# Performance work log

Measured on AMD Instinct MI355X. Metric: run time of the kernel, lower is better.

The kernel has to match this reference:

```python
import jax, jax.numpy as jnp
import numpy as np

C = 256
CQK = C // 8  # query/key channel dim from Conv3d(in, in//8, 1)


def setup_inputs() -> dict:
    key = jax.random.key(0)
    ks = jax.random.split(key, 8)
    B, D, H, W = 2, 16, 16, 16
    x = jax.random.normal(ks[0], (B, C, D, H, W), dtype=jnp.float32)
    s = 1.0 / np.sqrt(C)
    q_w = jax.random.normal(ks[1], (CQK, C), dtype=jnp.float32) * s
    q_b = jax.random.normal(ks[2], (CQK,), dtype=jnp.float32) * 0.01
    k_w = jax.random.normal(ks[3], (CQK, C), dtype=jnp.float32) * s
    k_b = jax.random.normal(ks[4], (CQK,), dtype=jnp.float32) * 0.01
    v_w = jax.random.normal(ks[5], (C, C), dtype=jnp.float32) * s
    v_b = jax.random.normal(ks[6], (C,), dtype=jnp.float32) * 0.01
    gamma = jax.random.normal(ks[7], (1,), dtype=jnp.float32)
    return {"x": x, "q_w": q_w, "q_b": q_b, "k_w": k_w, "k_b": k_b,
            "v_w": v_w, "v_b": v_b, "gamma": gamma}


def reference(x, q_w, q_b, k_w, k_b, v_w, v_b, gamma):
    B, Cc, D, H, W = x.shape
    N = D * H * W
    xf = x.reshape(B, Cc, N)  # [B, C, N]
    # 1x1x1 Conv3d == channel-mixing matmul
    q = jnp.einsum('oc,bcn->bon', q_w, xf) + q_b[None, :, None]  # [B, C/8, N]
    k = jnp.einsum('oc,bcn->bon', k_w, xf) + k_b[None, :, None]  # [B, C/8, N]
    v = jnp.einsum('oc,bcn->bon', v_w, xf) + v_b[None, :, None]  # [B, C, N]
    # attention[b, i, j] = sum_c q[b, c, i] * k[b, c, j]
    attn = jnp.einsum('bci,bcj->bij', q, k)  # [B, N, N]
    attn = jax.nn.softmax(attn, axis=-1)
    # out[b, c, i] = sum_j v[b, c, j] * attn[b, i, j]
    out = jnp.einsum('bcj,bij->bci', v, attn)  # [B, C, N]
    out = out.reshape(B, Cc, D, H, W)
    return gamma[0] * out + x
```

## Files before the change

kernel.cpp:

```cpp
#include <hip/hip_runtime.h>

#define C_DIM 256
#define CQK   32
#define N_DIM 4096
#define B_DIM 2

typedef __attribute__((ext_vector_type(8))) short bf16x8;
typedef __attribute__((ext_vector_type(4))) float f32x4;

__device__ __forceinline__ unsigned short f2bf(float f) {
    union { float f; unsigned u; } v; v.f = f;
    unsigned r = v.u + 0x7FFFu + ((v.u >> 16) & 1u);
    return (unsigned short)(r >> 16);
}
__device__ __forceinline__ unsigned pk2(float a, float b) {
    return (unsigned)f2bf(a) | ((unsigned)f2bf(b) << 16);
}
#define MFMA(A, B, C) __builtin_amdgcn_mfma_f32_16x16x32_bf16((A), (B), (C), 0, 0, 0)

__global__ __launch_bounds__(256) void wconv(
    const float* __restrict__ q_w, const float* __restrict__ q_b,
    const float* __restrict__ k_w, const float* __restrict__ k_b,
    const float* __restrict__ v_w, const float* __restrict__ v_b,
    unsigned short* __restrict__ wbf, float* __restrict__ biasf)
{
    int o = blockIdx.x, c = threadIdx.x;
    float w;
    if (o < 32)       w = q_w[o * C_DIM + c];
    else if (o < 64)  w = k_w[(o - 32) * C_DIM + c];
    else              w = v_w[(o - 64) * C_DIM + c];
    wbf[o * C_DIM + c] = f2bf(w);
    if (c == 0) biasf[o] = (o < 32) ? q_b[o] : (o < 64) ? k_b[o - 32] : v_b[o - 64];
}

__global__ __launch_bounds__(256, 2) void qkv_proj(
    const float* __restrict__ x, const unsigned short* __restrict__ wbf,
    const float* __restrict__ biasf,
    unsigned short* __restrict__ qT, unsigned short* __restrict__ kT,
    unsigned short* __restrict__ vbf)
{
    __shared__ __align__(16) unsigned short xsT[16 * 264];
    __shared__ __align__(16) unsigned short qkbuf[2][16 * 36];
    __shared__ __align__(16) unsigned short vbb[256 * 20];
    const int t  = threadIdx.x;
    const int b  = blockIdx.x >> 8;
    const int n0 = (blockIdx.x & 255) * 16;

    {
        int n4 = t & 3, cq = t >> 2;
        const float* xp = x + ((size_t)(b * C_DIM + cq * 4)) * N_DIM + n0 + n4 * 4;
        float4 r0 = *(const float4*)xp;
        float4 r1 = *(const float4*)(xp + N_DIM);
        float4 r2 = *(const float4*)(xp + 2 * N_DIM);
        float4 r3 = *(const float4*)(xp + 3 * N_DIM);
        float a0[4], a1[4], a2[4], a3[4];
        *(float4*)a0 = r0; *(float4*)a1 = r1; *(float4*)a2 = r2; *(float4*)a3 = r3;
        #pragma unroll
        for (int k = 0; k < 4; ++k) {
            uint2 pw;
            pw.x = pk2(a0[k], a1[k]);
            pw.y = pk2(a2[k], a3[k]);
            *(uint2*)&xsT[(n4 * 4 + k) * 264 + cq * 4] = pw;
        }
    }
    __syncthreads();

    const int w = t >> 6, lid = t & 63, lr = lid & 15, lq = lid >> 4;
    f32x4 acc[5] = {};
    #pragma unroll
    for (int ks = 0; ks < 8; ++ks) {
        bf16x8 xb = *(const bf16x8*)&xsT[lr * 264 + ks * 32 + lq * 8];
        #pragma unroll
        for (int u = 0; u < 5; ++u) {
            int gm = w * 5 + u;
            bf16x8 af = *(const bf16x8*)&wbf[(gm * 16 + lr) * C_DIM + ks * 32 + lq * 8];
            acc[u] = MFMA(af, xb, acc[u]);
        }
    }
    #pragma unroll
    for (int u = 0; u < 5; ++u) {
        int gm = w * 5 + u;
        float bv[4];
        *(float4*)bv = *(const float4*)&biasf[gm * 16 + lq * 4];
        if (gm >= 4) {
            int vc = (gm - 4) * 16 + lq * 4;
            #pragma unroll
            for (int r = 0; r < 4; ++r)
                vbb[(vc + r) * 20 + lr] = f2bf(acc[u][r] + bv[r]);
        } else {
            int sel = gm >> 1, half = gm & 1;
            uint2 pw;
            pw.x = pk2(acc[u][0] + bv[0], acc[u][1] + bv[1]);
            pw.y = pk2(acc[u][2] + bv[2], acc[u][3] + bv[3]);
            *(uint2*)&qkbuf[sel][lr * 36 + half * 16 + lq * 4] = pw;
        }
    }
    __syncthreads();
    if (t < 128) {
        int sel = t >> 6, idx = t & 63;
        int n = idx >> 2, ch8 = (idx & 3) * 8;
        const unsigned short* src = &qkbuf[sel][n * 36 + ch8];
        uint2 a = *(const uint2*)src;
        uint2 c = *(const uint2*)(src + 4);
        unsigned short* dst = (sel ? kT : qT) + ((size_t)b * N_DIM + n0 + n) * CQK + ch8;
        uint4 st; st.x = a.x; st.y = a.y; st.z = c.x; st.w = c.y;
        *(uint4*)dst = st;
    }
    {
        const unsigned short* src = &vbb[t * 20];
        uint2 a = *(const uint2*)(src + 0);
        uint2 bq = *(const uint2*)(src + 4);
        uint2 c = *(const uint2*)(src + 8);
        uint2 d = *(const uint2*)(src + 12);
        unsigned short* dst = vbf + ((size_t)b * C_DIM + t) * N_DIM + n0;
        uint4 s0; s0.x = a.x; s0.y = a.y; s0.z = bq.x; s0.w = bq.y;
        uint4 s1; s1.x = c.x; s1.y = c.y; s1.z = d.x; s1.w = d.y;
        *(uint4*)dst = s0;
        *(uint4*)(dst + 8) = s1;
    }
}

__global__ __launch_bounds__(256, 2) void attn_kernel(
    const unsigned short* __restrict__ qT, const unsigned short* __restrict__ kT,
    const unsigned short* __restrict__ vbf, const float* __restrict__ x,
    const float* __restrict__ gamma, float* __restrict__ out)
{
    __shared__ __align__(16) char smem[20480 + 1280];
    unsigned short* pbase = (unsigned short*)smem;
    float* obuf = (float*)smem;
    float* lbuf = (float*)(smem + 20480);

    const int t  = threadIdx.x;
    const int b  = blockIdx.x >> 8;
    const int qt = (blockIdx.x >> 2) & 63;
    const int cs = blockIdx.x & 3;
    const int i0 = qt * 64, c0 = cs * 64;
    const int w = t >> 6, lid = t & 63, lr = lid & 15, lq = lid >> 4;

    const unsigned short* qTb = qT + (size_t)b * N_DIM * CQK;
    const unsigned short* kTb = kT + (size_t)b * N_DIM * CQK;
    const unsigned short* vb  = vbf + (size_t)b * C_DIM * N_DIM;

    unsigned short* pW = pbase + w * (64 * 40);

    bf16x8 bq[4];
    #pragma unroll
    for (int it = 0; it < 4; ++it)
        bq[it] = *(const bf16x8*)&qTb[(i0 + it * 16 + lr) * CQK + lq * 8];

    f32x4 oa[4][4] = {};
    float lp[4] = {};

    const int jwbase = w * 1024;
    #pragma unroll 2
    for (int jj = 0; jj < 1024; jj += 32) {
        const int j0 = jwbase + jj;
        bf16x8 ak0 = *(const bf16x8*)&kTb[(j0 + lr) * CQK + lq * 8];
        bf16x8 ak1 = *(const bf16x8*)&kTb[(j0 + 16 + lr) * CQK + lq * 8];
        bf16x8 av[4];
        #pragma unroll
        for (int ct = 0; ct < 4; ++ct)
            av[ct] = *(const bf16x8*)&vb[(size_t)(c0 + ct * 16 + lr) * N_DIM + j0 + lq * 8];

        const f32x4 z = {};
        #pragma unroll
        for (int it = 0; it < 4; ++it) {
            f32x4 s0 = MFMA(ak0, bq[it], z);
            f32x4 s1 = MFMA(ak1, bq[it], z);
            float e0 = __expf(s0[0]), e1 = __expf(s0[1]), e2 = __expf(s0[2]), e3 = __expf(s0[3]);
            float f0 = __expf(s1[0]), f1 = __expf(s1[1]), f2 = __expf(s1[2]), f3 = __expf(s1[3]);
            lp[it] += ((e0 + e1) + (e2 + e3)) + ((f0 + f1) + (f2 + f3));
            uint2 pw0; pw0.x = pk2(e0, e1); pw0.y = pk2(e2, e3);
            uint2 pw1; pw1.x = pk2(f0, f1); pw1.y = pk2(f2, f3);
            unsigned short* prow = pW + (it * 16 + lr) * 40;
            *(uint2*)&prow[lq * 4]      = pw0;
            *(uint2*)&prow[16 + lq * 4] = pw1;
        }
        __asm__ __volatile__("" ::: "memory");
        #pragma unroll
        for (int it = 0; it < 4; ++it) {
            bf16x8 bp = *(const bf16x8*)&pW[(it * 16 + lr) * 40 + lq * 8];
            #pragma unroll
            for (int ct = 0; ct < 4; ++ct)
                oa[ct][it] = MFMA(av[ct], bp, oa[ct][it]);
        }
    }

    #pragma unroll
    for (int it = 0; it < 4; ++it) {
        lp[it] += __shfl_xor(lp[it], 16);
        lp[it] += __shfl_xor(lp[it], 32);
    }
    if (lq == 0) {
        #pragma unroll
        for (int it = 0; it < 4; ++it)
            lbuf[w * 64 + it * 16 + lr] = lp[it];
    }
    __syncthreads();

    for (int ph = 0; ph < 4; ++ph) {
        if (w == ph) {
            #pragma unroll
            for (int ct = 0; ct < 4; ++ct)
                #pragma unroll
                for (int it = 0; it < 4; ++it)
                    #pragma unroll
                    for (int r = 0; r < 4; ++r) {
                        int addr = (ct * 16 + lq * 4 + r) * 68 + it * 16 + lr;
                        if (ph == 0) obuf[addr]  = oa[ct][it][r];
                        else         obuf[addr] += oa[ct][it][r];
                    }
        }
        __syncthreads();
    }
    if (t < 64) {
        float l = lbuf[t] + lbuf[64 + t] + lbuf[128 + t] + lbuf[192 + t];
        lbuf[256 + t] = 1.f / l;
    }
    __syncthreads();

    const float g = gamma[0];
    const int cc = t >> 2;
    const int ic = (t & 3) * 16;
    const size_t rowbase = ((size_t)b * C_DIM + c0 + cc) * N_DIM + i0 + ic;
    #pragma unroll
    for (int k = 0; k < 4; ++k) {
        float4 ov4 = *(const float4*)&obuf[cc * 68 + ic + k * 4];
        float4 li  = *(const float4*)&lbuf[256 + ic + k * 4];
        float4 xv  = *(const float4*)(x + rowbase + k * 4);
        float4 ov;
        ov.x = g * ov4.x * li.x + xv.x;
        ov.y = g * ov4.y * li.y + xv.y;
        ov.z = g * ov4.z * li.z + xv.z;
        ov.w = g * ov4.w * li.w + xv.w;
        *(float4*)(out + rowbase + k * 4) = ov;
    }
}

extern "C" void kernel_launch(void* const* d_in, const int* in_sizes, int n_in,
                              void* d_out, int out_size, void* d_ws, size_t ws_size,
                              hipStream_t stream) {
    const float* x     = (const float*)d_in[0];
    const float* q_w   = (const float*)d_in[1];
    const float* q_b   = (const float*)d_in[2];
    const float* k_w   = (const float*)d_in[3];
    const float* k_b   = (const float*)d_in[4];
    const float* v_w   = (const float*)d_in[5];
    const float* v_b   = (const float*)d_in[6];
    const float* gamma = (const float*)d_in[7];
    float* out = (float*)d_out;

    char* ws = (char*)d_ws;
    unsigned short* qT    = (unsigned short*)(ws);
    unsigned short* kT    = (unsigned short*)(ws + 524288);
    unsigned short* vbf   = (unsigned short*)(ws + 1048576);
    unsigned short* wbf   = (unsigned short*)(ws + 5242880);
    float*          biasf = (float*)(ws + 5406720);

    hipLaunchKernelGGL(wconv, dim3(320), dim3(256), 0, stream,
                       q_w, q_b, k_w, k_b, v_w, v_b, wbf, biasf);
    hipLaunchKernelGGL(qkv_proj, dim3(B_DIM * 256), dim3(256), 0, stream,
                       x, wbf, biasf, qT, kT, vbf);
    hipLaunchKernelGGL(attn_kernel, dim3(B_DIM * 64 * 4), dim3(256), 0, stream,
                       qT, kT, vbf, x, gamma, out);
}
```

Before: 137.7 us.

## Prefetch next K/V tiles, fold log2e into Q weights, truncate bf16 packing

Scales the Q projection weights and bias by log2(e) so the attention loop can use the hardware exp2 instead of expf. It also packs the probabilities to bf16 by truncating with a single perm instruction instead of round-to-nearest arithmetic. The K and V fragment loads are software-pipelined one iteration ahead so global latency overlaps the MFMA and exp work. The costs are more live registers, a small loss of rounding accuracy in P, and one redundant wrapped-around prefetch on the last iteration.

```diff
diff --git a/kernel.cpp b/kernel.cpp
--- a/kernel.cpp
+++ b/kernel.cpp
@@ -16,6 +16,11 @@
 __device__ __forceinline__ unsigned pk2(float a, float b) {
     return (unsigned)f2bf(a) | ((unsigned)f2bf(b) << 16);
 }
+__device__ __forceinline__ unsigned pk2t(float a, float b) {
+    union { float f; unsigned u; } ua, ub; ua.f = a; ub.f = b;
+    return __builtin_amdgcn_perm(ub.u, ua.u, 0x07060302u);
+}
+#define EXP2(x) __builtin_amdgcn_exp2f(x)
 #define MFMA(A, B, C) __builtin_amdgcn_mfma_f32_16x16x32_bf16((A), (B), (C), 0, 0, 0)
 
 __global__ __launch_bounds__(256) void wconv(
@@ -24,13 +29,15 @@
     const float* __restrict__ v_w, const float* __restrict__ v_b,
     unsigned short* __restrict__ wbf, float* __restrict__ biasf)
 {
+    const float LOG2E = 1.4426950408889634f;
     int o = blockIdx.x, c = threadIdx.x;
     float w;
-    if (o < 32)       w = q_w[o * C_DIM + c];
+    if (o < 32)       w = q_w[o * C_DIM + c] * LOG2E;
     else if (o < 64)  w = k_w[(o - 32) * C_DIM + c];
     else              w = v_w[(o - 64) * C_DIM + c];
     wbf[o * C_DIM + c] = f2bf(w);
-    if (c == 0) biasf[o] = (o < 32) ? q_b[o] : (o < 64) ? k_b[o - 32] : v_b[o - 64];
+    if (c == 0) biasf[o] = (o < 32) ? q_b[o] * LOG2E
+                         : (o < 64) ? k_b[o - 32] : v_b[o - 64];
 }
 
 __global__ __launch_bounds__(256, 2) void qkv_proj(
@@ -152,26 +159,33 @@
     float lp[4] = {};
 
     const int jwbase = w * 1024;
+    bf16x8 ak0 = *(const bf16x8*)&kTb[(jwbase + lr) * CQK + lq * 8];
+    bf16x8 ak1 = *(const bf16x8*)&kTb[(jwbase + 16 + lr) * CQK + lq * 8];
+    bf16x8 av[4];
+    #pragma unroll
+    for (int ct = 0; ct < 4; ++ct)
+        av[ct] = *(const bf16x8*)&vb[(size_t)(c0 + ct * 16 + lr) * N_DIM + jwbase + lq * 8];
+
     #pragma unroll 2
     for (int jj = 0; jj < 1024; jj += 32) {
-        const int j0 = jwbase + jj;
-        bf16x8 ak0 = *(const bf16x8*)&kTb[(j0 + lr) * CQK + lq * 8];
-        bf16x8 ak1 = *(const bf16x8*)&kTb[(j0 + 16 + lr) * CQK + lq * 8];
-        bf16x8 av[4];
+        const int jn = jwbase + ((jj + 32) & 1023);
+        bf16x8 ak0n = *(const bf16x8*)&kTb[(jn + lr) * CQK + lq * 8];
+        bf16x8 ak1n = *(const bf16x8*)&kTb[(jn + 16 + lr) * CQK + lq * 8];
+        bf16x8 avn[4];
         #pragma unroll
         for (int ct = 0; ct < 4; ++ct)
-            av[ct] = *(const bf16x8*)&vb[(size_t)(c0 + ct * 16 + lr) * N_DIM + j0 + lq * 8];
+            avn[ct] = *(const bf16x8*)&vb[(size_t)(c0 + ct * 16 + lr) * N_DIM + jn + lq * 8];
 
         const f32x4 z = {};
         #pragma unroll
         for (int it = 0; it < 4; ++it) {
             f32x4 s0 = MFMA(ak0, bq[it], z);
             f32x4 s1 = MFMA(ak1, bq[it], z);
-            float e0 = __expf(s0[0]), e1 = __expf(s0[1]), e2 = __expf(s0[2]), e3 = __expf(s0[3]);
-            float f0 = __expf(s1[0]), f1 = __expf(s1[1]), f2 = __expf(s1[2]), f3 = __expf(s1[3]);
+            float e0 = EXP2(s0[0]), e1 = EXP2(s0[1]), e2 = EXP2(s0[2]), e3 = EXP2(s0[3]);
+            float f0 = EXP2(s1[0]), f1 = EXP2(s1[1]), f2 = EXP2(s1[2]), f3 = EXP2(s1[3]);
             lp[it] += ((e0 + e1) + (e2 + e3)) + ((f0 + f1) + (f2 + f3));
-            uint2 pw0; pw0.x = pk2(e0, e1); pw0.y = pk2(e2, e3);
-            uint2 pw1; pw1.x = pk2(f0, f1); pw1.y = pk2(f2, f3);
+            uint2 pw0; pw0.x = pk2t(e0, e1); pw0.y = pk2t(e2, e3);
+            uint2 pw1; pw1.x = pk2t(f0, f1); pw1.y = pk2t(f2, f3);
             unsigned short* prow = pW + (it * 16 + lr) * 40;
             *(uint2*)&prow[lq * 4]      = pw0;
             *(uint2*)&prow[16 + lq * 4] = pw1;
@@ -184,6 +198,9 @@
             for (int ct = 0; ct < 4; ++ct)
                 oa[ct][it] = MFMA(av[ct], bp, oa[ct][it]);
         }
+        ak0 = ak0n; ak1 = ak1n;
+        #pragma unroll
+        for (int ct = 0; ct < 4; ++ct) av[ct] = avn[ct];
     }
 
     #pragma unroll
```

Result: faster. 134.4 us (-2.4%).
